# Kernel optimization log

Measured on AMD Instinct MI355X. Metric: run time of the kernel, lower is better.

Reference implementation:

```python
import jax, jax.numpy as jnp
import numpy as np

B, T, D = 4, 2048, 1024
H, KVH = 16, 4          # query heads, kv heads
HD = D // H             # head_dim = 64
R = 32                  # partial rope dims
ROPE_BASE = 10000.0
EPS = 1e-6


def rmsnorm(x, scale):
    # per-head RMSNorm over last dim, computed in fp32 like the torch code
    xf = x.astype(jnp.float32)
    norm = jax.lax.rsqrt(jnp.mean(xf * xf, axis=-1, keepdims=True) + EPS)
    return (xf * norm).astype(x.dtype) * scale


def apply_rope(x, cos, sin):
    # x: (B,T,H,HD); rotate first R dims, pass the rest through
    x_r, x_p = x[..., :R], x[..., R:]
    half = R // 2
    x1, x2 = x_r[..., :half], x_r[..., half:]
    rotated = jnp.concatenate([x1 * cos - x2 * sin, x1 * sin + x2 * cos], axis=-1)
    return jnp.concatenate([rotated, x_p], axis=-1)


def setup_inputs() -> dict:
    key = jax.random.key(0)
    ks = jax.random.split(key, 8)
    x = jax.random.normal(ks[0], (B, T, D), dtype=jnp.float32)
    # RoPE tables exactly as RotaryEmbedding.get_cos_sin
    inv_freq = 1.0 / (ROPE_BASE ** (jnp.arange(0, R, 2, dtype=jnp.float32) / R))
    t = jnp.arange(T, dtype=jnp.float32)
    freqs = jnp.outer(t, inv_freq)                      # (T, R/2)
    cos = jnp.cos(freqs)[None, :, None, :]              # (1,T,1,R/2)
    sin = jnp.sin(freqs)[None, :, None, :]
    s = 1.0 / np.sqrt(D)
    Wq = jax.random.normal(ks[1], (D, D), dtype=jnp.float32) * s
    Wk = jax.random.normal(ks[2], (KVH * HD, D), dtype=jnp.float32) * s
    Wv = jax.random.normal(ks[3], (KVH * HD, D), dtype=jnp.float32) * s
    Wo = jax.random.normal(ks[4], (D, D), dtype=jnp.float32) * s
    q_scale = jnp.ones((HD,), dtype=jnp.float32)
    k_scale = jnp.ones((HD,), dtype=jnp.float32)
    return {"x": x, "cos": cos, "sin": sin, "Wq": Wq, "Wk": Wk, "Wv": Wv,
            "Wo": Wo, "q_scale": q_scale, "k_scale": k_scale}


def reference(x, cos, sin, Wq, Wk, Wv, Wo, q_scale, k_scale):
    b, t, d = x.shape
    q = jnp.einsum('btd,ed->bte', x, Wq).reshape(b, t, H, HD)
    k = jnp.einsum('btd,ed->bte', x, Wk).reshape(b, t, KVH, HD)
    v = jnp.einsum('btd,ed->bte', x, Wv).reshape(b, t, KVH, HD)
    q = apply_rope(rmsnorm(q, q_scale), cos, sin)
    k = apply_rope(rmsnorm(k, k_scale), cos, sin)
    groups = H // KVH
    k = jnp.repeat(k, groups, axis=2)   # (b,t,H,HD), matches repeat_interleave dim=2
    v = jnp.repeat(v, groups, axis=2)
    q = q.transpose(0, 2, 1, 3)         # (b,H,t,HD)
    k = k.transpose(0, 2, 1, 3)
    v = v.transpose(0, 2, 1, 3)
    scores = jnp.einsum('bhqd,bhkd->bhqk', q, k) / np.sqrt(HD)
    causal = jnp.tril(jnp.ones((t, t), dtype=bool))
    scores = jnp.where(causal, scores, -jnp.inf)
    attn = jax.nn.softmax(scores, axis=-1)
    y = jnp.einsum('bhqk,bhkd->bhqd', attn, v)
    y = y.transpose(0, 2, 1, 3).reshape(b, t, d)
    return jnp.einsum('btd,ed->bte', y, Wo)
```

## Files before the change

### kernel.cpp

```cpp
#include <hip/hip_runtime.h>
#include <hip/hip_bf16.h>
#include <stdint.h>

typedef __attribute__((ext_vector_type(8)))  __bf16 bf16x8;
typedef __attribute__((ext_vector_type(4)))  float  f32x4;
typedef __attribute__((ext_vector_type(16))) float  f32x16;
typedef __hip_bfloat16 bf16_t;

#define T_SEQ 2048
#define D_MODEL 1024
#define N_HEADS 16
#define N_KV 4
#define HD 64
#define LDQKV 1536
#define KDIM 1024

__device__ inline void cvt16(const float4* __restrict__ g, int4* __restrict__ s) {
  float4 v0 = g[0], v1 = g[1], v2 = g[2], v3 = g[3];
  union { int4 i[2]; __hip_bfloat162 h[8]; } u;
  u.h[0] = __float22bfloat162_rn(make_float2(v0.x, v0.y));
  u.h[1] = __float22bfloat162_rn(make_float2(v0.z, v0.w));
  u.h[2] = __float22bfloat162_rn(make_float2(v1.x, v1.y));
  u.h[3] = __float22bfloat162_rn(make_float2(v1.z, v1.w));
  u.h[4] = __float22bfloat162_rn(make_float2(v2.x, v2.y));
  u.h[5] = __float22bfloat162_rn(make_float2(v2.z, v2.w));
  u.h[6] = __float22bfloat162_rn(make_float2(v3.x, v3.y));
  u.h[7] = __float22bfloat162_rn(make_float2(v3.z, v3.w));
  s[0] = u.i[0]; s[1] = u.i[1];
}

__device__ inline void storeC(bf16_t* p, float v) { *p = __float2bfloat16(v); }
__device__ inline void storeC(float* p, float v) { *p = v; }

__device__ inline void plswap(unsigned& a, unsigned& b) {
  asm volatile("v_permlane32_swap_b32 %0, %1" : "+v"(a), "+v"(b));
}

__device__ inline float fexp2(float x) {
  float r; asm("v_exp_f32 %0, %1" : "=v"(r) : "v"(x)); return r;
}
__device__ inline unsigned cvtpk(float lo, float hi) {
  unsigned r; asm("v_cvt_pk_bf16_f32 %0, %1, %2" : "=v"(r) : "v"(lo), "v"(hi));
  return r;
}

__device__ inline void gll16(const bf16_t* g, bf16_t* l) {
  __builtin_amdgcn_global_load_lds(
      (const __attribute__((address_space(1))) void*)g,
      (__attribute__((address_space(3))) void*)l, 16, 0, 0);
}

__global__ __launch_bounds__(256) void to_bf16(const float* __restrict__ s,
                                               bf16_t* __restrict__ d,
                                               const int n16) {
  const int i = blockIdx.x * 256 + threadIdx.x;
  if (i < n16) cvt16((const float4*)s + i * 4, (int4*)d + i * 2);
}

__global__ __launch_bounds__(256) void w_cvt(
    const float* __restrict__ Wq, const float* __restrict__ Wk,
    const float* __restrict__ Wv, const float* __restrict__ Wo,
    bf16_t* __restrict__ wqkvb, bf16_t* __restrict__ wob) {
  const int i = blockIdx.x * 256 + threadIdx.x;
  const float* s; bf16_t* d; int off;
  if (i < 65536)       { s = Wq; d = wqkvb;                off = i; }
  else if (i < 81920)  { s = Wk; d = wqkvb + 1024 * 1024;  off = i - 65536; }
  else if (i < 98304)  { s = Wv; d = wqkvb + 1280 * 1024;  off = i - 81920; }
  else                 { s = Wo; d = wob;                  off = i - 98304; }
  cvt16((const float4*)s + off * 4, (int4*)d + off * 2);
}

template <int MODE, typename CT>
__global__ __launch_bounds__(256) void gemm_bb(
    const bf16_t* __restrict__ A, const bf16_t* __restrict__ W,
    CT* __restrict__ C, const int ldC,
    const float* __restrict__ cosb, const float* __restrict__ sinb,
    const float* __restrict__ qs, const float* __restrict__ ks,
    bf16_t* __restrict__ v_t)
{
  __shared__ bf16_t As[128 * 32];
  __shared__ bf16_t Bs[128 * 32];
  const int tid = threadIdx.x;
  const int lane = tid & 63;
  const int wv = tid >> 6;
  const int wr = wv >> 1, wc = wv & 1;
  const int m0 = blockIdx.y * 128;
  const int n0 = blockIdx.x * 128;

  const int srow = lane >> 2;
  const int scol = (lane & 3) * 8;
  const bf16_t* gA = A + (size_t)(m0 + 32 * wv + srow) * KDIM + scol;
  const bf16_t* gB = W + (size_t)(n0 + 32 * wv + srow) * KDIM + scol;
  bf16_t* lA = As + wv * 1024;
  bf16_t* lB = Bs + wv * 1024;

  f32x4 acc[4][4];
#pragma unroll
  for (int m = 0; m < 4; ++m)
#pragma unroll
    for (int n = 0; n < 4; ++n)
      acc[m][n] = {0.f, 0.f, 0.f, 0.f};

  const int fr = lane & 15;
  const int fq = lane >> 4;

  for (int k0 = 0; k0 < KDIM; k0 += 32) {
    gll16(gA + k0, lA);
    gll16(gA + 16 * KDIM + k0, lA + 512);
    gll16(gB + k0, lB);
    gll16(gB + 16 * KDIM + k0, lB + 512);
    __syncthreads();
    bf16x8 af[4], bfv[4];
#pragma unroll
    for (int m = 0; m < 4; ++m)
      af[m] = *(const bf16x8*)(&As[(wr * 64 + m * 16 + fr) * 32 + fq * 8]);
#pragma unroll
    for (int n = 0; n < 4; ++n)
      bfv[n] = *(const bf16x8*)(&Bs[(wc * 64 + n * 16 + fr) * 32 + fq * 8]);
#pragma unroll
    for (int m = 0; m < 4; ++m)
#pragma unroll
      for (int n = 0; n < 4; ++n)
        acc[m][n] = __builtin_amdgcn_mfma_f32_16x16x32_bf16(af[m], bfv[n],
                                                            acc[m][n], 0, 0, 0);
    __syncthreads();
  }

  if (MODE == 0 || n0 < 1280) {
    if (MODE == 1) {
      const float* stab = (n0 < 1024) ? qs : ks;
      float sc0 = stab[fr], sc1 = stab[16 + fr], sc2 = stab[32 + fr], sc3 = stab[48 + fr];
#pragma unroll
      for (int m = 0; m < 4; ++m)
#pragma unroll
        for (int r = 0; r < 4; ++r) {
          const int row = m0 + wr * 64 + m * 16 + fq * 4 + r;
          const int t = row & (T_SEQ - 1);
          float ss = acc[m][0][r] * acc[m][0][r] + acc[m][1][r] * acc[m][1][r]
                   + acc[m][2][r] * acc[m][2][r] + acc[m][3][r] * acc[m][3][r];
          ss += __shfl_xor(ss, 1);
          ss += __shfl_xor(ss, 2);
          ss += __shfl_xor(ss, 4);
          ss += __shfl_xor(ss, 8);
          const float nrm = rsqrtf(ss * (1.f / 64.f) + 1e-6f);
          const float v0 = acc[m][0][r] * nrm * sc0;
          const float v1 = acc[m][1][r] * nrm * sc1;
          const float v2 = acc[m][2][r] * nrm * sc2;
          const float v3 = acc[m][3][r] * nrm * sc3;
          const float c = cosb[t * 16 + fr];
          const float s = sinb[t * 16 + fr];
          const float r0 = v0 * c - v1 * s;
          const float r1 = v0 * s + v1 * c;
          bf16_t* p = (bf16_t*)C + (size_t)row * ldC + n0 + wc * 64 + fr;
          p[0]  = __float2bfloat16(r0);
          p[16] = __float2bfloat16(r1);
          p[32] = __float2bfloat16(v2);
          p[48] = __float2bfloat16(v3);
        }
    } else {
#pragma unroll
      for (int m = 0; m < 4; ++m)
#pragma unroll
        for (int n = 0; n < 4; ++n)
#pragma unroll
          for (int r = 0; r < 4; ++r) {
            const int row = wr * 64 + m * 16 + fq * 4 + r;
            const int col = wc * 64 + n * 16 + fr;
            storeC(&C[(size_t)(m0 + row) * ldC + n0 + col], acc[m][n][r]);
          }
    }
  } else {
#pragma unroll
    for (int m = 0; m < 4; ++m) {
      const int row0 = m0 + wr * 64 + m * 16 + fq * 4;
      const int b = row0 >> 11, t0 = row0 & (T_SEQ - 1);
#pragma unroll
      for (int n = 0; n < 4; ++n) {
        const int vcol = n0 - 1280 + wc * 64 + n * 16 + fr;
        const int g = b * 4 + (vcol >> 6);
        const int d = vcol & 63;
        uint2 pk2;
        pk2.x = cvtpk(acc[m][n][0], acc[m][n][1]);
        pk2.y = cvtpk(acc[m][n][2], acc[m][n][3]);
        *(uint2*)(v_t + ((size_t)g * HD + d) * T_SEQ + t0) = pk2;
      }
    }
  }
}

__global__ __launch_bounds__(256) void attn(
    const bf16_t* __restrict__ qkv, const bf16_t* __restrict__ v_t,
    bf16_t* __restrict__ y)
{
  __shared__ int4 lds[2048];
  const int tid  = threadIdx.x;
  const int lane = tid & 63;
  const int wv   = tid >> 6;
  const int ql   = lane & 31;
  const int hi   = lane >> 5;
  const int id   = (int)blockIdx.x;
  const int low3 = id & 7;
  const int rest = id >> 3;
  const int gsel = rest & 1;
  const int hh   = (rest >> 1) & 3;
  const int sbi  = rest >> 3;
  const int sb   = ((sbi >> 2) & 1) ? (sbi + 4 - ((sbi >> 3) << 4)) : (15 - sbi);
  const int g16  = low3 + 8 * gsel;
  const int b    = g16 >> 2, kvh = g16 & 3;
  const int h    = kvh * 4 + hh;
  const int s    = sb * 4 + wv;
  const int q_glob = s * 32 + ql;
  const int nt     = s + 1;
  const int nR     = 2 * sb + 2;
  const float SCALE_LOG2 = 0.125f * 1.44269504089f;

  const int kr = tid >> 3, kslot = tid & 7;
  const int vd = tid >> 2, vslot = tid & 3;
  const bf16_t* gK = qkv + (size_t)(b * T_SEQ + kr) * LDQKV + 1024 + kvh * HD + kslot * 8;
  const bf16_t* gV = v_t + (size_t)((b * N_KV + kvh) * HD + vd) * T_SEQ + vslot * 8;
  const int wKidx = kr * 8 + (kslot ^ (kr & 7));
  const int wVidx = 512 + vd * 4 + (vslot ^ ((vd >> 1) & 3));

  int kridx[4];
#pragma unroll
  for (int c = 0; c < 4; ++c)
    kridx[c] = ql * 8 + ((2 * c + hi) ^ (ql & 7));
  const int vsw = (ql >> 1) & 3;
  const int v0idx = 512 + ql * 4 + (hi ^ vsw);
  const int v1idx = 512 + ql * 4 + ((2 + hi) ^ vsw);
  const int v2idx = 512 + (ql + 32) * 4 + (hi ^ vsw);
  const int v3idx = 512 + (ql + 32) * 4 + ((2 + hi) ^ vsw);

  const bf16_t* Qrow = qkv + (size_t)(b * T_SEQ + q_glob) * LDQKV + h * HD + hi * 8;
  bf16x8 qfrag[4];
#pragma unroll
  for (int c = 0; c < 4; ++c) {
    bf16x8 raw = *(const bf16x8*)(Qrow + c * 16);
    bf16x8 sc;
#pragma unroll
    for (int j = 0; j < 8; ++j)
      sc[j] = (__bf16)((float)raw[j] * SCALE_LOG2);
    qfrag[c] = sc;
  }

  union ob { unsigned u[4]; bf16x8 v; } onesf;
#pragma unroll
  for (int i = 0; i < 4; ++i) onesf.u[i] = 0x3F803F80u;

  f32x16 acc0, acc1, accL, zro;
#pragma unroll
  for (int i = 0; i < 16; ++i) { acc0[i] = 0.f; acc1[i] = 0.f; accL[i] = 0.f; zro[i] = 0.f; }
  float m_run = -1e30f;

  {
    int4 kA = *(const int4*)gK;
    int4 vA = *(const int4*)gV;
    int4 kB = *(const int4*)(gK + (size_t)32 * LDQKV);
    int4 vB = *(const int4*)(gV + 32);
    lds[wKidx] = kA;       lds[wVidx] = vA;
    lds[256 + wKidx] = kB; lds[256 + wVidx] = vB;
  }
  __syncthreads();

  int buf = 0;
  for (int r = 0; r < nR; ++r) {
    int4 kA, vA, kB, vB;
    const bool more = (r + 1 < nR);
    if (more) {
      const size_t kAdv = (size_t)(r + 1) * 64 * LDQKV;
      const int vAdv = (r + 1) * 64;
      kA = *(const int4*)(gK + kAdv);
      vA = *(const int4*)(gV + vAdv);
      kB = *(const int4*)(gK + kAdv + (size_t)32 * LDQKV);
      vB = *(const int4*)(gV + vAdv + 32);
    }

#pragma unroll
    for (int u = 0; u < 2; ++u) {
      const int t = 2 * r + u;
      if (t < nt) {
        const int k0 = t << 5;
        const bool masked = (t == nt - 1);
        const int base = buf * 1024 + u * 256;

        bf16x8 kf0 = *(const bf16x8*)&lds[base + kridx[0]];
        bf16x8 kf1 = *(const bf16x8*)&lds[base + kridx[1]];
        bf16x8 kf2 = *(const bf16x8*)&lds[base + kridx[2]];
        bf16x8 kf3 = *(const bf16x8*)&lds[base + kridx[3]];

        f32x16 st = __builtin_amdgcn_mfma_f32_32x32x16_bf16(kf0, qfrag[0], zro, 0, 0, 0);
        st = __builtin_amdgcn_mfma_f32_32x32x16_bf16(kf1, qfrag[1], st, 0, 0, 0);
        st = __builtin_amdgcn_mfma_f32_32x32x16_bf16(kf2, qfrag[2], st, 0, 0, 0);
        st = __builtin_amdgcn_mfma_f32_32x32x16_bf16(kf3, qfrag[3], st, 0, 0, 0);

        if (masked) {
#pragma unroll
          for (int rr = 0; rr < 16; ++rr) {
            const int kg = k0 + (rr & 3) + 8 * (rr >> 2) + 4 * hi;
            if (kg > q_glob) st[rr] = -1e30f;
          }
        }
        float m01 = fmaxf(fmaxf(st[0], st[1]), st[2]);
        float m02 = fmaxf(fmaxf(st[3], st[4]), st[5]);
        float m03 = fmaxf(fmaxf(st[6], st[7]), st[8]);
        float m04 = fmaxf(fmaxf(st[9], st[10]), st[11]);
        float m05 = fmaxf(fmaxf(st[12], st[13]), st[14]);
        float m06 = fmaxf(fmaxf(m01, m02), m03);
        float m07 = fmaxf(fmaxf(m04, m05), st[15]);
        const float bmax = fmaxf(m06, m07);
        if (__any(bmax > m_run + 8.f)) {
          const float rmax = fmaxf(bmax, __shfl_xor(bmax, 32));
          const float mnew = fmaxf(m_run, rmax);
          const float corr = fexp2(m_run - mnew);
#pragma unroll
          for (int i = 0; i < 16; ++i) { acc0[i] *= corr; acc1[i] *= corr; }
          accL[0] *= corr;
          m_run = mnew;
        }
        float pp[16];
#pragma unroll
        for (int rr = 0; rr < 16; ++rr) pp[rr] = fexp2(st[rr] - m_run);

        unsigned w[8];
#pragma unroll
        for (int i = 0; i < 8; ++i) w[i] = cvtpk(pp[2 * i], pp[2 * i + 1]);
        plswap(w[0], w[2]); plswap(w[1], w[3]);
        plswap(w[4], w[6]); plswap(w[5], w[7]);
        union fu { unsigned u[4]; bf16x8 v; };
        fu f1, f2;
        f1.u[0] = w[0]; f1.u[1] = w[1]; f1.u[2] = w[2]; f1.u[3] = w[3];
        f2.u[0] = w[4]; f2.u[1] = w[5]; f2.u[2] = w[6]; f2.u[3] = w[7];

        bf16x8 vf0 = *(const bf16x8*)&lds[base + v0idx];
        bf16x8 vf1 = *(const bf16x8*)&lds[base + v1idx];
        bf16x8 vf2 = *(const bf16x8*)&lds[base + v2idx];
        bf16x8 vf3 = *(const bf16x8*)&lds[base + v3idx];

        acc0 = __builtin_amdgcn_mfma_f32_32x32x16_bf16(vf0, f1.v, acc0, 0, 0, 0);
        acc0 = __builtin_amdgcn_mfma_f32_32x32x16_bf16(vf1, f2.v, acc0, 0, 0, 0);
        acc1 = __builtin_amdgcn_mfma_f32_32x32x16_bf16(vf2, f1.v, acc1, 0, 0, 0);
        acc1 = __builtin_amdgcn_mfma_f32_32x32x16_bf16(vf3, f2.v, acc1, 0, 0, 0);
        accL = __builtin_amdgcn_mfma_f32_32x32x16_bf16(onesf.v, f1.v, accL, 0, 0, 0);
        accL = __builtin_amdgcn_mfma_f32_32x32x16_bf16(onesf.v, f2.v, accL, 0, 0, 0);
      }
    }

    if (more) {
      const int nb = (buf ^ 1) * 1024;
      lds[nb + wKidx] = kA;       lds[nb + wVidx] = vA;
      lds[nb + 256 + wKidx] = kB; lds[nb + 256 + wVidx] = vB;
    }
    __syncthreads();
    buf ^= 1;
  }

  const float inv = 1.f / accL[0];
  bf16_t* yrow = y + (size_t)(b * T_SEQ + q_glob) * D_MODEL + h * HD;
#pragma unroll
  for (int gg = 0; gg < 4; ++gg) {
    uint2 o0, o1;
    o0.x = cvtpk(acc0[4 * gg + 0] * inv, acc0[4 * gg + 1] * inv);
    o0.y = cvtpk(acc0[4 * gg + 2] * inv, acc0[4 * gg + 3] * inv);
    o1.x = cvtpk(acc1[4 * gg + 0] * inv, acc1[4 * gg + 1] * inv);
    o1.y = cvtpk(acc1[4 * gg + 2] * inv, acc1[4 * gg + 3] * inv);
    *(uint2*)(yrow + 8 * gg + 4 * hi)      = o0;
    *(uint2*)(yrow + 32 + 8 * gg + 4 * hi) = o1;
  }
}

extern "C" void kernel_launch(void* const* d_in, const int* in_sizes, int n_in,
                              void* d_out, int out_size, void* d_ws,
                              size_t ws_size, hipStream_t stream) {
  const float* x    = (const float*)d_in[0];
  const float* cosb = (const float*)d_in[1];
  const float* sinb = (const float*)d_in[2];
  const float* Wq   = (const float*)d_in[3];
  const float* Wk   = (const float*)d_in[4];
  const float* Wv   = (const float*)d_in[5];
  const float* Wo   = (const float*)d_in[6];
  const float* qs   = (const float*)d_in[7];
  const float* ks   = (const float*)d_in[8];
  float* out = (float*)d_out;

  char* ws = (char*)d_ws;
  bf16_t* qkv   = (bf16_t*)ws;
  bf16_t* v_t   = (bf16_t*)(ws + 25165824);
  bf16_t* y     = (bf16_t*)(ws + 29360128);
  bf16_t* xb    = y;
  bf16_t* wqkvb = (bf16_t*)(ws + 46137344);
  bf16_t* wob   = (bf16_t*)(ws + 49283072);

  to_bf16<<<dim3(2048), 256, 0, stream>>>(x, xb, 524288);
  w_cvt<<<dim3(640), 256, 0, stream>>>(Wq, Wk, Wv, Wo, wqkvb, wob);

  gemm_bb<1, bf16_t><<<dim3(12, 64), 256, 0, stream>>>(
      xb, wqkvb, qkv, LDQKV, cosb, sinb, qs, ks, v_t);
  attn<<<dim3(1024), 256, 0, stream>>>(qkv, v_t, y);
  gemm_bb<0, float><<<dim3(8, 64), 256, 0, stream>>>(
      y, wob, out, D_MODEL, nullptr, nullptr, nullptr, nullptr, nullptr);
}
```

Baseline: 166.7 us.

## Restructure attention into 2-wave blocks processing paired causal strips for balance

The attention kernel now uses 128-thread blocks (two waves) and 2048 blocks. Each block handles a pair of query strips, s and 63-s, one after the other, so every block does a near-equal amount of causal work. The KV tile per stage shrinks to 32 keys with a smaller LDS buffer. This replaces the old sb-permutation balancing and is meant to even out load and raise occupancy. The cost is more barriers per key and a reload of K/V tiles for the second strip, since the two waves share no tiles across strips.

```diff
diff --git a/kernel.cpp b/kernel.cpp
--- a/kernel.cpp
+++ b/kernel.cpp
@@ -188,11 +188,11 @@
   }
 }
 
-__global__ __launch_bounds__(256) void attn(
+__global__ __launch_bounds__(128) void attn(
     const bf16_t* __restrict__ qkv, const bf16_t* __restrict__ v_t,
     bf16_t* __restrict__ y)
 {
-  __shared__ int4 lds[2048];
+  __shared__ int4 lds[1024];
   const int tid  = threadIdx.x;
   const int lane = tid & 63;
   const int wv   = tid >> 6;
@@ -203,85 +203,97 @@
   const int rest = id >> 3;
   const int gsel = rest & 1;
   const int hh   = (rest >> 1) & 3;
-  const int sbi  = rest >> 3;
-  const int sb   = ((sbi >> 2) & 1) ? (sbi + 4 - ((sbi >> 3) << 4)) : (15 - sbi);
+  const int p    = rest >> 3;
   const int g16  = low3 + 8 * gsel;
   const int b    = g16 >> 2, kvh = g16 & 3;
   const int h    = kvh * 4 + hh;
-  const int s    = sb * 4 + wv;
-  const int q_glob = s * 32 + ql;
-  const int nt     = s + 1;
-  const int nR     = 2 * sb + 2;
+  const int sA   = 2 * p + wv;
   const float SCALE_LOG2 = 0.125f * 1.44269504089f;
 
-  const int kr = tid >> 3, kslot = tid & 7;
-  const int vd = tid >> 2, vslot = tid & 3;
-  const bf16_t* gK = qkv + (size_t)(b * T_SEQ + kr) * LDQKV + 1024 + kvh * HD + kslot * 8;
-  const bf16_t* gV = v_t + (size_t)((b * N_KV + kvh) * HD + vd) * T_SEQ + vslot * 8;
-  const int wKidx = kr * 8 + (kslot ^ (kr & 7));
-  const int wVidx = 512 + vd * 4 + (vslot ^ ((vd >> 1) & 3));
+  const int ks1 = tid + 128;
+  const int kr0 = tid >> 3, kc0 = tid & 7;
+  const int kr1 = ks1 >> 3, kc1 = ks1 & 7;
+  const bf16_t* gK0 = qkv + (size_t)(b * T_SEQ + kr0) * LDQKV + 1024 + kvh * HD + kc0 * 8;
+  const bf16_t* gK1 = qkv + (size_t)(b * T_SEQ + kr1) * LDQKV + 1024 + kvh * HD + kc1 * 8;
+  const int wK0 = kr0 * 8 + (kc0 ^ (kr0 & 7));
+  const int wK1 = kr1 * 8 + (kc1 ^ (kr1 & 7));
+  const int vd0 = tid >> 2, vc0 = tid & 3;
+  const int vs1 = tid + 128;
+  const int vd1 = vs1 >> 2, vc1 = vs1 & 3;
+  const bf16_t* gV0 = v_t + (size_t)((b * N_KV + kvh) * HD + vd0) * T_SEQ + vc0 * 8;
+  const bf16_t* gV1 = v_t + (size_t)((b * N_KV + kvh) * HD + vd1) * T_SEQ + vc1 * 8;
+  const int wV0 = 256 + vd0 * 4 + (vc0 ^ ((vd0 >> 1) & 3));
+  const int wV1 = 256 + vd1 * 4 + (vc1 ^ ((vd1 >> 1) & 3));
 
   int kridx[4];
 #pragma unroll
   for (int c = 0; c < 4; ++c)
     kridx[c] = ql * 8 + ((2 * c + hi) ^ (ql & 7));
   const int vsw = (ql >> 1) & 3;
-  const int v0idx = 512 + ql * 4 + (hi ^ vsw);
-  const int v1idx = 512 + ql * 4 + ((2 + hi) ^ vsw);
-  const int v2idx = 512 + (ql + 32) * 4 + (hi ^ vsw);
-  const int v3idx = 512 + (ql + 32) * 4 + ((2 + hi) ^ vsw);
-
-  const bf16_t* Qrow = qkv + (size_t)(b * T_SEQ + q_glob) * LDQKV + h * HD + hi * 8;
-  bf16x8 qfrag[4];
-#pragma unroll
-  for (int c = 0; c < 4; ++c) {
-    bf16x8 raw = *(const bf16x8*)(Qrow + c * 16);
-    bf16x8 sc;
-#pragma unroll
-    for (int j = 0; j < 8; ++j)
-      sc[j] = (__bf16)((float)raw[j] * SCALE_LOG2);
-    qfrag[c] = sc;
-  }
+  const int v0idx = 256 + ql * 4 + (hi ^ vsw);
+  const int v1idx = 256 + ql * 4 + ((2 + hi) ^ vsw);
+  const int v2idx = 256 + (ql + 32) * 4 + (hi ^ vsw);
+  const int v3idx = 256 + (ql + 32) * 4 + ((2 + hi) ^ vsw);
 
   union ob { unsigned u[4]; bf16x8 v; } onesf;
 #pragma unroll
   for (int i = 0; i < 4; ++i) onesf.u[i] = 0x3F803F80u;
 
-  f32x16 acc0, acc1, accL, zro;
-#pragma unroll
-  for (int i = 0; i < 16; ++i) { acc0[i] = 0.f; acc1[i] = 0.f; accL[i] = 0.f; zro[i] = 0.f; }
-  float m_run = -1e30f;
-
-  {
-    int4 kA = *(const int4*)gK;
-    int4 vA = *(const int4*)gV;
-    int4 kB = *(const int4*)(gK + (size_t)32 * LDQKV);
-    int4 vB = *(const int4*)(gV + 32);
-    lds[wKidx] = kA;       lds[wVidx] = vA;
-    lds[256 + wKidx] = kB; lds[256 + wVidx] = vB;
-  }
-  __syncthreads();
+  f32x16 zro;
+#pragma unroll
+  for (int i = 0; i < 16; ++i) zro[i] = 0.f;
 
   int buf = 0;
-  for (int r = 0; r < nR; ++r) {
-    int4 kA, vA, kB, vB;
-    const bool more = (r + 1 < nR);
-    if (more) {
-      const size_t kAdv = (size_t)(r + 1) * 64 * LDQKV;
-      const int vAdv = (r + 1) * 64;
-      kA = *(const int4*)(gK + kAdv);
-      vA = *(const int4*)(gV + vAdv);
-      kB = *(const int4*)(gK + kAdv + (size_t)32 * LDQKV);
-      vB = *(const int4*)(gV + vAdv + 32);
-    }
-
-#pragma unroll
-    for (int u = 0; u < 2; ++u) {
-      const int t = 2 * r + u;
+#pragma unroll
+  for (int pi = 0; pi < 2; ++pi) {
+    const int s = pi ? (63 - sA) : sA;
+    const int q_glob = s * 32 + ql;
+    const int nt = s + 1;
+    const int ntmax = pi ? (64 - 2 * p) : (2 * p + 2);
+
+    const bf16_t* Qrow = qkv + (size_t)(b * T_SEQ + q_glob) * LDQKV + h * HD + hi * 8;
+    bf16x8 qfrag[4];
+#pragma unroll
+    for (int c = 0; c < 4; ++c) {
+      bf16x8 raw = *(const bf16x8*)(Qrow + c * 16);
+      bf16x8 sc;
+#pragma unroll
+      for (int j = 0; j < 8; ++j)
+        sc[j] = (__bf16)((float)raw[j] * SCALE_LOG2);
+      qfrag[c] = sc;
+    }
+
+    f32x16 acc0, acc1, accL;
+#pragma unroll
+    for (int i = 0; i < 16; ++i) { acc0[i] = 0.f; acc1[i] = 0.f; accL[i] = 0.f; }
+    float m_run = -1e30f;
+
+    {
+      int4 a0 = *(const int4*)gK0; int4 a1 = *(const int4*)gK1;
+      int4 a2 = *(const int4*)gV0; int4 a3 = *(const int4*)gV1;
+      const int nb = buf * 512;
+      lds[nb + wK0] = a0; lds[nb + wK1] = a1;
+      lds[nb + wV0] = a2; lds[nb + wV1] = a3;
+    }
+    __syncthreads();
+
+    const bf16_t* pK0 = gK0 + (size_t)32 * LDQKV;
+    const bf16_t* pK1 = gK1 + (size_t)32 * LDQKV;
+    const bf16_t* pV0 = gV0 + 32;
+    const bf16_t* pV1 = gV1 + 32;
+
+    for (int t = 0; t < ntmax; ++t) {
+      int4 a0, a1, a2, a3;
+      const bool more = (t + 1 < ntmax);
+      if (more) {
+        a0 = *(const int4*)pK0; a1 = *(const int4*)pK1;
+        a2 = *(const int4*)pV0; a3 = *(const int4*)pV1;
+      }
+
       if (t < nt) {
         const int k0 = t << 5;
         const bool masked = (t == nt - 1);
-        const int base = buf * 1024 + u * 256;
+        const int base = buf * 512;
 
         bf16x8 kf0 = *(const bf16x8*)&lds[base + kridx[0]];
         bf16x8 kf1 = *(const bf16x8*)&lds[base + kridx[1]];
@@ -343,28 +355,30 @@
         accL = __builtin_amdgcn_mfma_f32_32x32x16_bf16(onesf.v, f1.v, accL, 0, 0, 0);
         accL = __builtin_amdgcn_mfma_f32_32x32x16_bf16(onesf.v, f2.v, accL, 0, 0, 0);
       }
-    }
-
-    if (more) {
-      const int nb = (buf ^ 1) * 1024;
-      lds[nb + wKidx] = kA;       lds[nb + wVidx] = vA;
-      lds[nb + 256 + wKidx] = kB; lds[nb + 256 + wVidx] = vB;
-    }
-    __syncthreads();
-    buf ^= 1;
-  }
-
-  const float inv = 1.f / accL[0];
-  bf16_t* yrow = y + (size_t)(b * T_SEQ + q_glob) * D_MODEL + h * HD;
-#pragma unroll
-  for (int gg = 0; gg < 4; ++gg) {
-    uint2 o0, o1;
-    o0.x = cvtpk(acc0[4 * gg + 0] * inv, acc0[4 * gg + 1] * inv);
-    o0.y = cvtpk(acc0[4 * gg + 2] * inv, acc0[4 * gg + 3] * inv);
-    o1.x = cvtpk(acc1[4 * gg + 0] * inv, acc1[4 * gg + 1] * inv);
-    o1.y = cvtpk(acc1[4 * gg + 2] * inv, acc1[4 * gg + 3] * inv);
-    *(uint2*)(yrow + 8 * gg + 4 * hi)      = o0;
-    *(uint2*)(yrow + 32 + 8 * gg + 4 * hi) = o1;
+
+      if (more) {
+        const int nb = (buf ^ 1) * 512;
+        lds[nb + wK0] = a0; lds[nb + wK1] = a1;
+        lds[nb + wV0] = a2; lds[nb + wV1] = a3;
+        pK0 += (size_t)32 * LDQKV; pK1 += (size_t)32 * LDQKV;
+        pV0 += 32; pV1 += 32;
+      }
+      __syncthreads();
+      buf ^= 1;
+    }
+
+    const float inv = 1.f / accL[0];
+    bf16_t* yrow = y + (size_t)(b * T_SEQ + q_glob) * D_MODEL + h * HD;
+#pragma unroll
+    for (int gg = 0; gg < 4; ++gg) {
+      uint2 o0, o1;
+      o0.x = cvtpk(acc0[4 * gg + 0] * inv, acc0[4 * gg + 1] * inv);
+      o0.y = cvtpk(acc0[4 * gg + 2] * inv, acc0[4 * gg + 3] * inv);
+      o1.x = cvtpk(acc1[4 * gg + 0] * inv, acc1[4 * gg + 1] * inv);
+      o1.y = cvtpk(acc1[4 * gg + 2] * inv, acc1[4 * gg + 3] * inv);
+      *(uint2*)(yrow + 8 * gg + 4 * hi)      = o0;
+      *(uint2*)(yrow + 32 + 8 * gg + 4 * hi) = o1;
+    }
   }
 }
 
@@ -395,7 +409,7 @@
 
   gemm_bb<1, bf16_t><<<dim3(12, 64), 256, 0, stream>>>(
       xb, wqkvb, qkv, LDQKV, cosb, sinb, qs, ks, v_t);
-  attn<<<dim3(1024), 256, 0, stream>>>(qkv, v_t, y);
+  attn<<<dim3(2048), 128, 0, stream>>>(qkv, v_t, y);
   gemm_bb<0, float><<<dim3(8, 64), 256, 0, stream>>>(
       y, wob, out, D_MODEL, nullptr, nullptr, nullptr, nullptr, nullptr);
 }
```

After: 240.2 us. 44.1% more time.

## Pair causal attention strips per block, merge conversion kernels, add MFMA priority

Applied to the files above, without the earlier changes.

Each attention block now handles two complementary query strips (s and 63-s), so every block does the same amount of causal work and the grid halves to 512 blocks. This replaces the earlier heuristic block ordering. The input and weight bf16 conversions are merged into one launch to save launch overhead, and s_setprio is raised around the MFMA groups to favour matrix issue. The risk is that fewer blocks lowers occupancy and leaves less latency hiding on a 256-CU part.

```diff
diff --git a/kernel.cpp b/kernel.cpp
--- a/kernel.cpp
+++ b/kernel.cpp
@@ -50,23 +50,19 @@
       (__attribute__((address_space(3))) void*)l, 16, 0, 0);
 }
 
-__global__ __launch_bounds__(256) void to_bf16(const float* __restrict__ s,
-                                               bf16_t* __restrict__ d,
-                                               const int n16) {
-  const int i = blockIdx.x * 256 + threadIdx.x;
-  if (i < n16) cvt16((const float4*)s + i * 4, (int4*)d + i * 2);
-}
-
-__global__ __launch_bounds__(256) void w_cvt(
+__global__ __launch_bounds__(256) void all_cvt(
+    const float* __restrict__ x,
     const float* __restrict__ Wq, const float* __restrict__ Wk,
     const float* __restrict__ Wv, const float* __restrict__ Wo,
-    bf16_t* __restrict__ wqkvb, bf16_t* __restrict__ wob) {
+    bf16_t* __restrict__ xb, bf16_t* __restrict__ wqkvb,
+    bf16_t* __restrict__ wob) {
   const int i = blockIdx.x * 256 + threadIdx.x;
   const float* s; bf16_t* d; int off;
-  if (i < 65536)       { s = Wq; d = wqkvb;                off = i; }
-  else if (i < 81920)  { s = Wk; d = wqkvb + 1024 * 1024;  off = i - 65536; }
-  else if (i < 98304)  { s = Wv; d = wqkvb + 1280 * 1024;  off = i - 81920; }
-  else                 { s = Wo; d = wob;                  off = i - 98304; }
+  if (i < 524288)      { s = x;  d = xb;                   off = i; }
+  else if (i < 589824) { s = Wq; d = wqkvb;                off = i - 524288; }
+  else if (i < 606208) { s = Wk; d = wqkvb + 1024 * 1024;  off = i - 589824; }
+  else if (i < 622592) { s = Wv; d = wqkvb + 1280 * 1024;  off = i - 606208; }
+  else                 { s = Wo; d = wob;                  off = i - 622592; }
   cvt16((const float4*)s + off * 4, (int4*)d + off * 2);
 }
 
@@ -203,15 +199,11 @@
   const int rest = id >> 3;
   const int gsel = rest & 1;
   const int hh   = (rest >> 1) & 3;
-  const int sbi  = rest >> 3;
-  const int sb   = ((sbi >> 2) & 1) ? (sbi + 4 - ((sbi >> 3) << 4)) : (15 - sbi);
+  const int p    = rest >> 3;
   const int g16  = low3 + 8 * gsel;
   const int b    = g16 >> 2, kvh = g16 & 3;
   const int h    = kvh * 4 + hh;
-  const int s    = sb * 4 + wv;
-  const int q_glob = s * 32 + ql;
-  const int nt     = s + 1;
-  const int nR     = 2 * sb + 2;
+  const int sA   = 4 * p + wv;
   const float SCALE_LOG2 = 0.125f * 1.44269504089f;
 
   const int kr = tid >> 3, kslot = tid & 7;
@@ -231,140 +223,157 @@
   const int v2idx = 512 + (ql + 32) * 4 + (hi ^ vsw);
   const int v3idx = 512 + (ql + 32) * 4 + ((2 + hi) ^ vsw);
 
-  const bf16_t* Qrow = qkv + (size_t)(b * T_SEQ + q_glob) * LDQKV + h * HD + hi * 8;
-  bf16x8 qfrag[4];
-#pragma unroll
-  for (int c = 0; c < 4; ++c) {
-    bf16x8 raw = *(const bf16x8*)(Qrow + c * 16);
-    bf16x8 sc;
-#pragma unroll
-    for (int j = 0; j < 8; ++j)
-      sc[j] = (__bf16)((float)raw[j] * SCALE_LOG2);
-    qfrag[c] = sc;
-  }
-
   union ob { unsigned u[4]; bf16x8 v; } onesf;
 #pragma unroll
   for (int i = 0; i < 4; ++i) onesf.u[i] = 0x3F803F80u;
 
-  f32x16 acc0, acc1, accL, zro;
-#pragma unroll
-  for (int i = 0; i < 16; ++i) { acc0[i] = 0.f; acc1[i] = 0.f; accL[i] = 0.f; zro[i] = 0.f; }
-  float m_run = -1e30f;
-
-  {
-    int4 kA = *(const int4*)gK;
-    int4 vA = *(const int4*)gV;
-    int4 kB = *(const int4*)(gK + (size_t)32 * LDQKV);
-    int4 vB = *(const int4*)(gV + 32);
-    lds[wKidx] = kA;       lds[wVidx] = vA;
-    lds[256 + wKidx] = kB; lds[256 + wVidx] = vB;
-  }
-  __syncthreads();
+  f32x16 zro;
+#pragma unroll
+  for (int i = 0; i < 16; ++i) zro[i] = 0.f;
 
   int buf = 0;
-  for (int r = 0; r < nR; ++r) {
-    int4 kA, vA, kB, vB;
-    const bool more = (r + 1 < nR);
-    if (more) {
-      const size_t kAdv = (size_t)(r + 1) * 64 * LDQKV;
-      const int vAdv = (r + 1) * 64;
-      kA = *(const int4*)(gK + kAdv);
-      vA = *(const int4*)(gV + vAdv);
-      kB = *(const int4*)(gK + kAdv + (size_t)32 * LDQKV);
-      vB = *(const int4*)(gV + vAdv + 32);
-    }
-
-#pragma unroll
-    for (int u = 0; u < 2; ++u) {
-      const int t = 2 * r + u;
-      if (t < nt) {
-        const int k0 = t << 5;
-        const bool masked = (t == nt - 1);
-        const int base = buf * 1024 + u * 256;
-
-        bf16x8 kf0 = *(const bf16x8*)&lds[base + kridx[0]];
-        bf16x8 kf1 = *(const bf16x8*)&lds[base + kridx[1]];
-        bf16x8 kf2 = *(const bf16x8*)&lds[base + kridx[2]];
-        bf16x8 kf3 = *(const bf16x8*)&lds[base + kridx[3]];
-
-        f32x16 st = __builtin_amdgcn_mfma_f32_32x32x16_bf16(kf0, qfrag[0], zro, 0, 0, 0);
-        st = __builtin_amdgcn_mfma_f32_32x32x16_bf16(kf1, qfrag[1], st, 0, 0, 0);
-        st = __builtin_amdgcn_mfma_f32_32x32x16_bf16(kf2, qfrag[2], st, 0, 0, 0);
-        st = __builtin_amdgcn_mfma_f32_32x32x16_bf16(kf3, qfrag[3], st, 0, 0, 0);
-
-        if (masked) {
-#pragma unroll
-          for (int rr = 0; rr < 16; ++rr) {
-            const int kg = k0 + (rr & 3) + 8 * (rr >> 2) + 4 * hi;
-            if (kg > q_glob) st[rr] = -1e30f;
-          }
-        }
-        float m01 = fmaxf(fmaxf(st[0], st[1]), st[2]);
-        float m02 = fmaxf(fmaxf(st[3], st[4]), st[5]);
-        float m03 = fmaxf(fmaxf(st[6], st[7]), st[8]);
-        float m04 = fmaxf(fmaxf(st[9], st[10]), st[11]);
-        float m05 = fmaxf(fmaxf(st[12], st[13]), st[14]);
-        float m06 = fmaxf(fmaxf(m01, m02), m03);
-        float m07 = fmaxf(fmaxf(m04, m05), st[15]);
-        const float bmax = fmaxf(m06, m07);
-        if (__any(bmax > m_run + 8.f)) {
-          const float rmax = fmaxf(bmax, __shfl_xor(bmax, 32));
-          const float mnew = fmaxf(m_run, rmax);
-          const float corr = fexp2(m_run - mnew);
-#pragma unroll
-          for (int i = 0; i < 16; ++i) { acc0[i] *= corr; acc1[i] *= corr; }
-          accL[0] *= corr;
-          m_run = mnew;
-        }
-        float pp[16];
-#pragma unroll
-        for (int rr = 0; rr < 16; ++rr) pp[rr] = fexp2(st[rr] - m_run);
-
-        unsigned w[8];
-#pragma unroll
-        for (int i = 0; i < 8; ++i) w[i] = cvtpk(pp[2 * i], pp[2 * i + 1]);
-        plswap(w[0], w[2]); plswap(w[1], w[3]);
-        plswap(w[4], w[6]); plswap(w[5], w[7]);
-        union fu { unsigned u[4]; bf16x8 v; };
-        fu f1, f2;
-        f1.u[0] = w[0]; f1.u[1] = w[1]; f1.u[2] = w[2]; f1.u[3] = w[3];
-        f2.u[0] = w[4]; f2.u[1] = w[5]; f2.u[2] = w[6]; f2.u[3] = w[7];
-
-        bf16x8 vf0 = *(const bf16x8*)&lds[base + v0idx];
-        bf16x8 vf1 = *(const bf16x8*)&lds[base + v1idx];
-        bf16x8 vf2 = *(const bf16x8*)&lds[base + v2idx];
-        bf16x8 vf3 = *(const bf16x8*)&lds[base + v3idx];
-
-        acc0 = __builtin_amdgcn_mfma_f32_32x32x16_bf16(vf0, f1.v, acc0, 0, 0, 0);
-        acc0 = __builtin_amdgcn_mfma_f32_32x32x16_bf16(vf1, f2.v, acc0, 0, 0, 0);
-        acc1 = __builtin_amdgcn_mfma_f32_32x32x16_bf16(vf2, f1.v, acc1, 0, 0, 0);
-        acc1 = __builtin_amdgcn_mfma_f32_32x32x16_bf16(vf3, f2.v, acc1, 0, 0, 0);
-        accL = __builtin_amdgcn_mfma_f32_32x32x16_bf16(onesf.v, f1.v, accL, 0, 0, 0);
-        accL = __builtin_amdgcn_mfma_f32_32x32x16_bf16(onesf.v, f2.v, accL, 0, 0, 0);
-      }
-    }
-
-    if (more) {
-      const int nb = (buf ^ 1) * 1024;
+#pragma unroll
+  for (int pi = 0; pi < 2; ++pi) {
+    const int s = pi ? (63 - sA) : sA;
+    const int q_glob = s * 32 + ql;
+    const int nt = s + 1;
+    const int nR = pi ? (32 - 2 * p) : (2 * p + 2);
+
+    const bf16_t* Qrow = qkv + (size_t)(b * T_SEQ + q_glob) * LDQKV + h * HD + hi * 8;
+    bf16x8 qfrag[4];
+#pragma unroll
+    for (int c = 0; c < 4; ++c) {
+      bf16x8 raw = *(const bf16x8*)(Qrow + c * 16);
+      bf16x8 sc;
+#pragma unroll
+      for (int j = 0; j < 8; ++j)
+        sc[j] = (__bf16)((float)raw[j] * SCALE_LOG2);
+      qfrag[c] = sc;
+    }
+
+    f32x16 acc0, acc1, accL;
+#pragma unroll
+    for (int i = 0; i < 16; ++i) { acc0[i] = 0.f; acc1[i] = 0.f; accL[i] = 0.f; }
+    float m_run = -1e30f;
+
+    {
+      int4 kA = *(const int4*)gK;
+      int4 vA = *(const int4*)gV;
+      int4 kB = *(const int4*)(gK + (size_t)32 * LDQKV);
+      int4 vB = *(const int4*)(gV + 32);
+      const int nb = buf * 1024;
       lds[nb + wKidx] = kA;       lds[nb + wVidx] = vA;
       lds[nb + 256 + wKidx] = kB; lds[nb + 256 + wVidx] = vB;
     }
     __syncthreads();
-    buf ^= 1;
-  }
-
-  const float inv = 1.f / accL[0];
-  bf16_t* yrow = y + (size_t)(b * T_SEQ + q_glob) * D_MODEL + h * HD;
-#pragma unroll
-  for (int gg = 0; gg < 4; ++gg) {
-    uint2 o0, o1;
-    o0.x = cvtpk(acc0[4 * gg + 0] * inv, acc0[4 * gg + 1] * inv);
-    o0.y = cvtpk(acc0[4 * gg + 2] * inv, acc0[4 * gg + 3] * inv);
-    o1.x = cvtpk(acc1[4 * gg + 0] * inv, acc1[4 * gg + 1] * inv);
-    o1.y = cvtpk(acc1[4 * gg + 2] * inv, acc1[4 * gg + 3] * inv);
-    *(uint2*)(yrow + 8 * gg + 4 * hi)      = o0;
-    *(uint2*)(yrow + 32 + 8 * gg + 4 * hi) = o1;
+
+    for (int r = 0; r < nR; ++r) {
+      int4 kA, vA, kB, vB;
+      const bool more = (r + 1 < nR);
+      if (more) {
+        const size_t kAdv = (size_t)(r + 1) * 64 * LDQKV;
+        const int vAdv = (r + 1) * 64;
+        kA = *(const int4*)(gK + kAdv);
+        vA = *(const int4*)(gV + vAdv);
+        kB = *(const int4*)(gK + kAdv + (size_t)32 * LDQKV);
+        vB = *(const int4*)(gV + vAdv + 32);
+      }
+
+#pragma unroll
+      for (int u = 0; u < 2; ++u) {
+        const int t = 2 * r + u;
+        if (t < nt) {
+          const int k0 = t << 5;
+          const bool masked = (t == nt - 1);
+          const int base = buf * 1024 + u * 256;
+
+          bf16x8 kf0 = *(const bf16x8*)&lds[base + kridx[0]];
+          bf16x8 kf1 = *(const bf16x8*)&lds[base + kridx[1]];
+          bf16x8 kf2 = *(const bf16x8*)&lds[base + kridx[2]];
+          bf16x8 kf3 = *(const bf16x8*)&lds[base + kridx[3]];
+
+          __builtin_amdgcn_s_setprio(1);
+          f32x16 st = __builtin_amdgcn_mfma_f32_32x32x16_bf16(kf0, qfrag[0], zro, 0, 0, 0);
+          st = __builtin_amdgcn_mfma_f32_32x32x16_bf16(kf1, qfrag[1], st, 0, 0, 0);
+          st = __builtin_amdgcn_mfma_f32_32x32x16_bf16(kf2, qfrag[2], st, 0, 0, 0);
+          st = __builtin_amdgcn_mfma_f32_32x32x16_bf16(kf3, qfrag[3], st, 0, 0, 0);
+          __builtin_amdgcn_s_setprio(0);
+
+          if (masked) {
+#pragma unroll
+            for (int rr = 0; rr < 16; ++rr) {
+              const int kg = k0 + (rr & 3) + 8 * (rr >> 2) + 4 * hi;
+              if (kg > q_glob) st[rr] = -1e30f;
+            }
+          }
+          float m01 = fmaxf(fmaxf(st[0], st[1]), st[2]);
+          float m02 = fmaxf(fmaxf(st[3], st[4]), st[5]);
+          float m03 = fmaxf(fmaxf(st[6], st[7]), st[8]);
+          float m04 = fmaxf(fmaxf(st[9], st[10]), st[11]);
+          float m05 = fmaxf(fmaxf(st[12], st[13]), st[14]);
+          float m06 = fmaxf(fmaxf(m01, m02), m03);
+          float m07 = fmaxf(fmaxf(m04, m05), st[15]);
+          const float bmax = fmaxf(m06, m07);
+          if (__any(bmax > m_run + 8.f)) {
+            const float rmax = fmaxf(bmax, __shfl_xor(bmax, 32));
+            const float mnew = fmaxf(m_run, rmax);
+            const float corr = fexp2(m_run - mnew);
+#pragma unroll
+            for (int i = 0; i < 16; ++i) { acc0[i] *= corr; acc1[i] *= corr; }
+            accL[0] *= corr;
+            m_run = mnew;
+          }
+          float pp[16];
+#pragma unroll
+          for (int rr = 0; rr < 16; ++rr) pp[rr] = fexp2(st[rr] - m_run);
+
+          unsigned w[8];
+#pragma unroll
+          for (int i = 0; i < 8; ++i) w[i] = cvtpk(pp[2 * i], pp[2 * i + 1]);
+          plswap(w[0], w[2]); plswap(w[1], w[3]);
+          plswap(w[4], w[6]); plswap(w[5], w[7]);
+          union fu { unsigned u[4]; bf16x8 v; };
+          fu f1, f2;
+          f1.u[0] = w[0]; f1.u[1] = w[1]; f1.u[2] = w[2]; f1.u[3] = w[3];
+          f2.u[0] = w[4]; f2.u[1] = w[5]; f2.u[2] = w[6]; f2.u[3] = w[7];
+
+          bf16x8 vf0 = *(const bf16x8*)&lds[base + v0idx];
+          bf16x8 vf1 = *(const bf16x8*)&lds[base + v1idx];
+          bf16x8 vf2 = *(const bf16x8*)&lds[base + v2idx];
+          bf16x8 vf3 = *(const bf16x8*)&lds[base + v3idx];
+
+          __builtin_amdgcn_s_setprio(1);
+          acc0 = __builtin_amdgcn_mfma_f32_32x32x16_bf16(vf0, f1.v, acc0, 0, 0, 0);
+          acc0 = __builtin_amdgcn_mfma_f32_32x32x16_bf16(vf1, f2.v, acc0, 0, 0, 0);
+          acc1 = __builtin_amdgcn_mfma_f32_32x32x16_bf16(vf2, f1.v, acc1, 0, 0, 0);
+          acc1 = __builtin_amdgcn_mfma_f32_32x32x16_bf16(vf3, f2.v, acc1, 0, 0, 0);
+          accL = __builtin_amdgcn_mfma_f32_32x32x16_bf16(onesf.v, f1.v, accL, 0, 0, 0);
+          accL = __builtin_amdgcn_mfma_f32_32x32x16_bf16(onesf.v, f2.v, accL, 0, 0, 0);
+          __builtin_amdgcn_s_setprio(0);
+        }
+      }
+
+      if (more) {
+        const int nb = (buf ^ 1) * 1024;
+        lds[nb + wKidx] = kA;       lds[nb + wVidx] = vA;
+        lds[nb + 256 + wKidx] = kB; lds[nb + 256 + wVidx] = vB;
+      }
+      __syncthreads();
+      buf ^= 1;
+    }
+
+    const float inv = 1.f / accL[0];
+    bf16_t* yrow = y + (size_t)(b * T_SEQ + q_glob) * D_MODEL + h * HD;
+#pragma unroll
+    for (int gg = 0; gg < 4; ++gg) {
+      uint2 o0, o1;
+      o0.x = cvtpk(acc0[4 * gg + 0] * inv, acc0[4 * gg + 1] * inv);
+      o0.y = cvtpk(acc0[4 * gg + 2] * inv, acc0[4 * gg + 3] * inv);
+      o1.x = cvtpk(acc1[4 * gg + 0] * inv, acc1[4 * gg + 1] * inv);
+      o1.y = cvtpk(acc1[4 * gg + 2] * inv, acc1[4 * gg + 3] * inv);
+      *(uint2*)(yrow + 8 * gg + 4 * hi)      = o0;
+      *(uint2*)(yrow + 32 + 8 * gg + 4 * hi) = o1;
+    }
   }
 }
 
@@ -390,12 +399,11 @@
   bf16_t* wqkvb = (bf16_t*)(ws + 46137344);
   bf16_t* wob   = (bf16_t*)(ws + 49283072);
 
-  to_bf16<<<dim3(2048), 256, 0, stream>>>(x, xb, 524288);
-  w_cvt<<<dim3(640), 256, 0, stream>>>(Wq, Wk, Wv, Wo, wqkvb, wob);
+  all_cvt<<<dim3(2688), 256, 0, stream>>>(x, Wq, Wk, Wv, Wo, xb, wqkvb, wob);
 
   gemm_bb<1, bf16_t><<<dim3(12, 64), 256, 0, stream>>>(
       xb, wqkvb, qkv, LDQKV, cosb, sinb, qs, ks, v_t);
-  attn<<<dim3(1024), 256, 0, stream>>>(qkv, v_t, y);
+  attn<<<dim3(512), 256, 0, stream>>>(qkv, v_t, y);
   gemm_bb<0, float><<<dim3(8, 64), 256, 0, stream>>>(
       y, wob, out, D_MODEL, nullptr, nullptr, nullptr, nullptr, nullptr);
 }
```

Result: faster. 163.3 us (-2.0%).
